# Kernel optimization log

Hardware: AMD Instinct MI355X
Metric: run time of the kernel (lower is better)

The kernel has to match this reference:

```python
import jax, jax.numpy as jnp
import numpy as np

N_NODES = 8192
DIM = 512

def setup_inputs() -> dict:
    key = jax.random.key(0)
    k1, k2, k3, k4 = jax.random.split(key, 4)
    x = jax.random.normal(k1, (N_NODES, DIM), dtype=jnp.float32)
    adj = jax.random.uniform(k2, (N_NODES, N_NODES), dtype=jnp.float32)
    # nn.Linear(dim, dim): weight [out, in], bias [out]
    bound = 1.0 / np.sqrt(DIM)
    W = jax.random.uniform(k3, (DIM, DIM), minval=-bound, maxval=bound, dtype=jnp.float32)
    b = jax.random.uniform(k4, (DIM,), minval=-bound, maxval=bound, dtype=jnp.float32)
    return {"x": x, "adj": adj, "W": W, "b": b}

def reference(x, adj, W, b):
    # agg = adj @ x : [N, dim]
    agg = jnp.matmul(adj, x)
    # Linear: agg @ W.T + b, then ReLU
    out = jnp.matmul(agg, W.T) + b
    return jax.nn.relu(out)
```

## Files before the change

kernel.cpp:

```cpp
#include <hip/hip_runtime.h>

typedef __bf16 bf16_t;
typedef bf16_t bf16x8 __attribute__((ext_vector_type(8)));
typedef bf16_t bf16x4 __attribute__((ext_vector_type(4)));
typedef float f32x4 __attribute__((ext_vector_type(4)));

#define N_NODES 8192
#define DIM 512

__global__ __launch_bounds__(256) void k_transpose_x(const float* __restrict__ x,
                                                     bf16_t* __restrict__ xT) {
  __shared__ float tile[64][65];
  const int m0 = blockIdx.x * 64;
  const int n0 = blockIdx.y * 64;
  const int t = threadIdx.x;
  const int r = t >> 4;
  const int c = (t & 15) << 2;
#pragma unroll
  for (int i = 0; i < 4; ++i) {
    f32x4 v = *(const f32x4*)&x[(size_t)(m0 + r + i * 16) * DIM + n0 + c];
    tile[r + i * 16][c + 0] = v.x;
    tile[r + i * 16][c + 1] = v.y;
    tile[r + i * 16][c + 2] = v.z;
    tile[r + i * 16][c + 3] = v.w;
  }
  __syncthreads();
#pragma unroll
  for (int i = 0; i < 4; ++i) {
    const int rn = r + i * 16;
    bf16x4 o = {(bf16_t)tile[c + 0][rn], (bf16_t)tile[c + 1][rn],
                (bf16_t)tile[c + 2][rn], (bf16_t)tile[c + 3][rn]};
    *(bf16x4*)&xT[(size_t)(n0 + rn) * N_NODES + m0 + c] = o;
  }
}

__global__ __launch_bounds__(256) void k_cvt_w(const float* __restrict__ W,
                                               bf16_t* __restrict__ Wb) {
  const int t = blockIdx.x * 256 + threadIdx.x;
  f32x4 v = *(const f32x4*)&W[(size_t)t * 4];
  bf16x4 o = {(bf16_t)v.x, (bf16_t)v.y, (bf16_t)v.z, (bf16_t)v.w};
  *(bf16x4*)&Wb[(size_t)t * 4] = o;
}

template <int S>
__global__ __launch_bounds__(512, 4) void k_gemm1(const float* __restrict__ A,
                                                  const bf16_t* __restrict__ Bt,
                                                  float* __restrict__ P) {
  constexpr int K = N_NODES;
  constexpr int KC = K / S;
  constexpr int NIT = KC / 32;
  constexpr int LD = 40;
  __shared__ bf16_t As[2][128 * LD];
  __shared__ bf16_t Bs[2][128 * LD];

  const int b = blockIdx.x;
  const int xcd = b & 7;
  const int i6 = b >> 3;
  const int n_tile = i6 & 3;
  const int s = (i6 >> 2) & (S - 1);
  const int mg = (i6 >> 2) / S;
  const int m0 = (mg * 8 + xcd) * 128;
  const int n0 = n_tile * 128;

  const int t = threadIdx.x;
  const int lane = t & 63;
  const int w = t >> 6;
  const int wr = w & 1;
  const int wc = w >> 1;
  const int lrow = lane & 15;
  const int quad = lane >> 4;
  const int sr = t >> 2;
  const int sq = t & 3;

  const float* ap = A + (size_t)(m0 + sr) * K + s * KC + sq * 8;
  const bf16_t* bp = Bt + (size_t)(n0 + sr) * K + s * KC + sq * 8;
  const int wofs = sr * LD + sq * 8;

  f32x4 pa0[2], pa1[2];
  bf16x8 pb[2];
  auto load_pre = [&](int k0, int sl) {
    pa0[sl] = *(const f32x4*)(ap + k0);
    pa1[sl] = *(const f32x4*)(ap + k0 + 4);
    pb[sl] = *(const bf16x8*)(bp + k0);
  };
  auto stage = [&](int sl, int buf) {
    bf16x8 av;
#pragma unroll
    for (int z = 0; z < 4; ++z) {
      av[z] = (bf16_t)pa0[sl][z];
      av[z + 4] = (bf16_t)pa1[sl][z];
    }
    *(bf16x8*)&As[buf][wofs] = av;
    *(bf16x8*)&Bs[buf][wofs] = pb[sl];
  };

  load_pre(0, 0);
  stage(0, 0);
  if (NIT > 1) load_pre(32, 1);
  f32x4 acc[4][2] = {};
  __syncthreads();

  int cur = 0;
#pragma unroll 2
  for (int it = 0; it < NIT; ++it) {
    if (it + 2 < NIT) load_pre((it + 2) * 32, it & 1);
    bf16x8 af[4], bfr[2];
#pragma unroll
    for (int ii = 0; ii < 4; ++ii)
      af[ii] = *(const bf16x8*)&As[cur][(wr * 64 + ii * 16 + lrow) * LD + quad * 8];
#pragma unroll
    for (int jj = 0; jj < 2; ++jj)
      bfr[jj] = *(const bf16x8*)&Bs[cur][(wc * 32 + jj * 16 + lrow) * LD + quad * 8];
#pragma unroll
    for (int ii = 0; ii < 4; ++ii)
#pragma unroll
      for (int jj = 0; jj < 2; ++jj)
        acc[ii][jj] = __builtin_amdgcn_mfma_f32_16x16x32_bf16(af[ii], bfr[jj], acc[ii][jj], 0, 0, 0);
    if (it + 1 < NIT) stage((it + 1) & 1, cur ^ 1);
    __syncthreads();
    cur ^= 1;
  }

  float* Pp = P + (size_t)s * N_NODES * DIM;
#pragma unroll
  for (int ii = 0; ii < 4; ++ii)
#pragma unroll
    for (int jj = 0; jj < 2; ++jj) {
      const int col = n0 + wc * 32 + jj * 16 + lrow;
#pragma unroll
      for (int r = 0; r < 4; ++r) {
        const int row = m0 + wr * 64 + ii * 16 + quad * 4 + r;
        Pp[(size_t)row * DIM + col] = acc[ii][jj][r];
      }
    }
}

template <int S>
__global__ __launch_bounds__(256, 2) void k_gemm2(const float* __restrict__ P,
                                                  const bf16_t* __restrict__ Bw,
                                                  const float* __restrict__ bias,
                                                  float* __restrict__ out) {
  constexpr int K = DIM;
  constexpr int LDA = 72;
  constexpr int LDB = 72;
  constexpr size_t PS = (size_t)N_NODES * DIM;
  __shared__ bf16_t As[64 * LDA];
  __shared__ bf16_t Bs[128 * LDB];

  const int b = blockIdx.x;
  const int n0 = (b & 3) * 128;
  const int m0 = (b >> 2) * 64;
  const int t = threadIdx.x;
  const int lane = t & 63;
  const int w = t >> 6;
  const int wr = w & 1;
  const int wc = w >> 1;
  const int lrow = lane & 15;
  const int quad = lane >> 4;
  const int ar = t >> 2, aq = t & 3;
  const int br = t >> 1, bq = t & 1;

  const float* ap = P + (size_t)(m0 + ar) * K + aq * 16;
  const bf16_t* bp = Bw + (size_t)(n0 + br) * K + bq * 32;
  bf16_t* aw = &As[ar * LDA + aq * 16];
  bf16_t* bw = &Bs[br * LDB + bq * 32];

  f32x4 acc[2][4] = {};

  for (int k0 = 0; k0 < K; k0 += 64) {
    f32x4 av[4];
#pragma unroll
    for (int z = 0; z < 4; ++z) av[z] = *(const f32x4*)(ap + k0 + z * 4);
#pragma unroll
    for (int s2 = 1; s2 < S; ++s2)
#pragma unroll
      for (int z = 0; z < 4; ++z) av[z] += *(const f32x4*)(ap + s2 * PS + k0 + z * 4);
    bf16x8 b0 = *(const bf16x8*)(bp + k0);
    bf16x8 b1 = *(const bf16x8*)(bp + k0 + 8);
    bf16x8 b2 = *(const bf16x8*)(bp + k0 + 16);
    bf16x8 b3 = *(const bf16x8*)(bp + k0 + 24);
    bf16x8 a0, a1;
#pragma unroll
    for (int z = 0; z < 4; ++z) {
      a0[z] = (bf16_t)av[0][z];
      a0[z + 4] = (bf16_t)av[1][z];
      a1[z] = (bf16_t)av[2][z];
      a1[z + 4] = (bf16_t)av[3][z];
    }
    __syncthreads();
    *(bf16x8*)aw = a0;
    *(bf16x8*)(aw + 8) = a1;
    *(bf16x8*)bw = b0;
    *(bf16x8*)(bw + 8) = b1;
    *(bf16x8*)(bw + 16) = b2;
    *(bf16x8*)(bw + 24) = b3;
    __syncthreads();
#pragma unroll
    for (int kk = 0; kk < 64; kk += 32) {
      bf16x8 af0 = *(const bf16x8*)&As[(wr * 32 + 0 + lrow) * LDA + kk + quad * 8];
      bf16x8 af1 = *(const bf16x8*)&As[(wr * 32 + 16 + lrow) * LDA + kk + quad * 8];
      bf16x8 bf0 = *(const bf16x8*)&Bs[(wc * 64 + 0 + lrow) * LDB + kk + quad * 8];
      bf16x8 bf1 = *(const bf16x8*)&Bs[(wc * 64 + 16 + lrow) * LDB + kk + quad * 8];
      bf16x8 bf2 = *(const bf16x8*)&Bs[(wc * 64 + 32 + lrow) * LDB + kk + quad * 8];
      bf16x8 bf3 = *(const bf16x8*)&Bs[(wc * 64 + 48 + lrow) * LDB + kk + quad * 8];
      acc[0][0] = __builtin_amdgcn_mfma_f32_16x16x32_bf16(af0, bf0, acc[0][0], 0, 0, 0);
      acc[0][1] = __builtin_amdgcn_mfma_f32_16x16x32_bf16(af0, bf1, acc[0][1], 0, 0, 0);
      acc[0][2] = __builtin_amdgcn_mfma_f32_16x16x32_bf16(af0, bf2, acc[0][2], 0, 0, 0);
      acc[0][3] = __builtin_amdgcn_mfma_f32_16x16x32_bf16(af0, bf3, acc[0][3], 0, 0, 0);
      acc[1][0] = __builtin_amdgcn_mfma_f32_16x16x32_bf16(af1, bf0, acc[1][0], 0, 0, 0);
      acc[1][1] = __builtin_amdgcn_mfma_f32_16x16x32_bf16(af1, bf1, acc[1][1], 0, 0, 0);
      acc[1][2] = __builtin_amdgcn_mfma_f32_16x16x32_bf16(af1, bf2, acc[1][2], 0, 0, 0);
      acc[1][3] = __builtin_amdgcn_mfma_f32_16x16x32_bf16(af1, bf3, acc[1][3], 0, 0, 0);
    }
  }

#pragma unroll
  for (int i = 0; i < 2; ++i)
#pragma unroll
    for (int j = 0; j < 4; ++j) {
      const int col = n0 + wc * 64 + j * 16 + lrow;
      const float bj = bias[col];
#pragma unroll
      for (int r = 0; r < 4; ++r) {
        const int row = m0 + wr * 32 + i * 16 + quad * 4 + r;
        float v = acc[i][j][r] + bj;
        out[(size_t)row * DIM + col] = v > 0.0f ? v : 0.0f;
      }
    }
}

extern "C" void kernel_launch(void* const* d_in, const int* in_sizes, int n_in,
                              void* d_out, int out_size, void* d_ws, size_t ws_size,
                              hipStream_t stream) {
  const float* x = (const float*)d_in[0];
  const float* adj = (const float*)d_in[1];
  const float* W = (const float*)d_in[2];
  const float* b = (const float*)d_in[3];
  float* out = (float*)d_out;

  bf16_t* xT = (bf16_t*)d_ws;
  bf16_t* Wb = xT + (size_t)DIM * N_NODES;
  float* P = (float*)(Wb + (size_t)DIM * DIM);
  const size_t base = (size_t)DIM * N_NODES * 2 + (size_t)DIM * DIM * 2;
  const size_t pslab = (size_t)N_NODES * DIM * 4;

  k_transpose_x<<<dim3(N_NODES / 64, DIM / 64), 256, 0, stream>>>(x, xT);
  k_cvt_w<<<dim3((DIM * DIM / 4) / 256), 256, 0, stream>>>(W, Wb);

  if (ws_size >= base + 4 * pslab) {
    k_gemm1<4><<<dim3(256 * 4), 512, 0, stream>>>(adj, xT, P);
    k_gemm2<4><<<dim3(512), 256, 0, stream>>>(P, Wb, b, out);
  } else {
    k_gemm1<1><<<dim3(256), 512, 0, stream>>>(adj, xT, P);
    k_gemm2<1><<<dim3(512), 256, 0, stream>>>(P, Wb, b, out);
  }
}
```

Baseline: 508.5 us.

## Stage gemm1 tiles via direct global-to-LDS loads with XOR swizzle and bigger warp tiles

```diff
diff --git a/kernel.cpp b/kernel.cpp
--- a/kernel.cpp
+++ b/kernel.cpp
@@ -1,4 +1,5 @@
 #include <hip/hip_runtime.h>
+#include <stdint.h>
 
 typedef __bf16 bf16_t;
 typedef bf16_t bf16x8 __attribute__((ext_vector_type(8)));
@@ -7,6 +8,13 @@
 
 #define N_NODES 8192
 #define DIM 512
+
+typedef __attribute__((address_space(1))) void as1_void;
+typedef __attribute__((address_space(3))) void as3_void;
+
+__device__ __forceinline__ void gload_lds16(const void* g, void* l) {
+  __builtin_amdgcn_global_load_lds((as1_void*)g, (as3_void*)l, 16, 0, 0);
+}
 
 __global__ __launch_bounds__(256) void k_transpose_x(const float* __restrict__ x,
                                                      bf16_t* __restrict__ xT) {
@@ -43,15 +51,14 @@
 }
 
 template <int S>
-__global__ __launch_bounds__(512, 4) void k_gemm1(const float* __restrict__ A,
+__global__ __launch_bounds__(256, 3) void k_gemm1(const float* __restrict__ A,
                                                   const bf16_t* __restrict__ Bt,
                                                   float* __restrict__ P) {
   constexpr int K = N_NODES;
   constexpr int KC = K / S;
   constexpr int NIT = KC / 32;
-  constexpr int LD = 40;
-  __shared__ bf16_t As[2][128 * LD];
-  __shared__ bf16_t Bs[2][128 * LD];
+  __shared__ float As[2][128 * 32];
+  __shared__ bf16_t Bs[2][128 * 32];
 
   const int b = blockIdx.x;
   const int xcd = b & 7;
@@ -69,64 +76,70 @@
   const int wc = w >> 1;
   const int lrow = lane & 15;
   const int quad = lane >> 4;
-  const int sr = t >> 2;
-  const int sq = t & 3;
-
-  const float* ap = A + (size_t)(m0 + sr) * K + s * KC + sq * 8;
-  const bf16_t* bp = Bt + (size_t)(n0 + sr) * K + s * KC + sq * 8;
-  const int wofs = sr * LD + sq * 8;
-
-  f32x4 pa0[2], pa1[2];
-  bf16x8 pb[2];
-  auto load_pre = [&](int k0, int sl) {
-    pa0[sl] = *(const f32x4*)(ap + k0);
-    pa1[sl] = *(const f32x4*)(ap + k0 + 4);
-    pb[sl] = *(const bf16x8*)(bp + k0);
+
+  const int aoff = ((t & 7) ^ ((t >> 3) & 7)) * 4;
+  const int boff = ((t & 3) ^ ((t >> 3) & 3)) * 8;
+  const float* ag = A + (size_t)(m0 + (t >> 3)) * K + (size_t)s * KC + aoff;
+  const bf16_t* bg = Bt + (size_t)(n0 + (t >> 2)) * K + (size_t)s * KC + boff;
+
+  auto stage = [&](int it, int buf) {
+    const int kc = it * 32;
+#pragma unroll
+    for (int i = 0; i < 4; ++i)
+      gload_lds16(ag + (size_t)(i * 32) * K + kc, &As[buf][(i * 256 + t) * 4]);
+#pragma unroll
+    for (int i = 0; i < 2; ++i)
+      gload_lds16(bg + (size_t)(i * 64) * K + kc, &Bs[buf][(i * 256 + t) * 8]);
   };
-  auto stage = [&](int sl, int buf) {
-    bf16x8 av;
-#pragma unroll
-    for (int z = 0; z < 4; ++z) {
-      av[z] = (bf16_t)pa0[sl][z];
-      av[z + 4] = (bf16_t)pa1[sl][z];
-    }
-    *(bf16x8*)&As[buf][wofs] = av;
-    *(bf16x8*)&Bs[buf][wofs] = pb[sl];
+
+  const int apc0 = ((quad * 2) ^ (lrow & 7)) * 4;
+  const int apc1 = (((quad * 2) ^ (lrow & 7)) ^ 1) * 4;
+  const int bpc = (quad ^ ((lrow >> 1) & 3)) * 8;
+
+  f32x4 acc[4][4] = {};
+
+  auto compute = [&](int buf) {
+    bf16x8 af[4], bfr[4];
+#pragma unroll
+    for (int ii = 0; ii < 4; ++ii) {
+      const int rb = (wr * 64 + ii * 16 + lrow) * 32;
+      f32x4 a0 = *(const f32x4*)&As[buf][rb + apc0];
+      f32x4 a1 = *(const f32x4*)&As[buf][rb + apc1];
+#pragma unroll
+      for (int z = 0; z < 4; ++z) {
+        af[ii][z] = (bf16_t)a0[z];
+        af[ii][z + 4] = (bf16_t)a1[z];
+      }
+    }
+#pragma unroll
+    for (int jj = 0; jj < 4; ++jj)
+      bfr[jj] = *(const bf16x8*)&Bs[buf][(wc * 64 + jj * 16 + lrow) * 32 + bpc];
+#pragma unroll
+    for (int ii = 0; ii < 4; ++ii)
+#pragma unroll
+      for (int jj = 0; jj < 4; ++jj)
+        acc[ii][jj] =
+            __builtin_amdgcn_mfma_f32_16x16x32_bf16(af[ii], bfr[jj], acc[ii][jj], 0, 0, 0);
   };
 
-  load_pre(0, 0);
   stage(0, 0);
-  if (NIT > 1) load_pre(32, 1);
-  f32x4 acc[4][2] = {};
   __syncthreads();
-
-  int cur = 0;
-#pragma unroll 2
-  for (int it = 0; it < NIT; ++it) {
-    if (it + 2 < NIT) load_pre((it + 2) * 32, it & 1);
-    bf16x8 af[4], bfr[2];
-#pragma unroll
-    for (int ii = 0; ii < 4; ++ii)
-      af[ii] = *(const bf16x8*)&As[cur][(wr * 64 + ii * 16 + lrow) * LD + quad * 8];
-#pragma unroll
-    for (int jj = 0; jj < 2; ++jj)
-      bfr[jj] = *(const bf16x8*)&Bs[cur][(wc * 32 + jj * 16 + lrow) * LD + quad * 8];
-#pragma unroll
-    for (int ii = 0; ii < 4; ++ii)
-#pragma unroll
-      for (int jj = 0; jj < 2; ++jj)
-        acc[ii][jj] = __builtin_amdgcn_mfma_f32_16x16x32_bf16(af[ii], bfr[jj], acc[ii][jj], 0, 0, 0);
-    if (it + 1 < NIT) stage((it + 1) & 1, cur ^ 1);
-    __syncthreads();
-    cur ^= 1;
+#pragma unroll 1
+  for (int it = 0; it < NIT; it += 2) {
+    stage(it + 1, 1);
+    compute(0);
+    __syncthreads();
+    if (it + 2 < NIT) stage(it + 2, 0);
+    compute(1);
+    __syncthreads();
   }
 
   float* Pp = P + (size_t)s * N_NODES * DIM;
 #pragma unroll
   for (int ii = 0; ii < 4; ++ii)
 #pragma unroll
-    for (int jj = 0; jj < 2; ++jj) {
-      const int col = n0 + wc * 32 + jj * 16 + lrow;
+    for (int jj = 0; jj < 4; ++jj) {
+      const int col = n0 + wc * 64 + jj * 16 + lrow;
 #pragma unroll
       for (int r = 0; r < 4; ++r) {
         const int row = m0 + wr * 64 + ii * 16 + quad * 4 + r;
@@ -148,8 +161,10 @@
   __shared__ bf16_t Bs[128 * LDB];
 
   const int b = blockIdx.x;
-  const int n0 = (b & 3) * 128;
-  const int m0 = (b >> 2) * 64;
+  const int xcd = b & 7;
+  const int j = b >> 3;
+  const int n0 = (j & 3) * 128;
+  const int m0 = ((j >> 2) * 8 + xcd) * 64;
   const int t = threadIdx.x;
   const int lane = t & 63;
   const int w = t >> 6;
@@ -217,13 +232,13 @@
 #pragma unroll
   for (int i = 0; i < 2; ++i)
 #pragma unroll
-    for (int j = 0; j < 4; ++j) {
-      const int col = n0 + wc * 64 + j * 16 + lrow;
+    for (int j2 = 0; j2 < 4; ++j2) {
+      const int col = n0 + wc * 64 + j2 * 16 + lrow;
       const float bj = bias[col];
 #pragma unroll
       for (int r = 0; r < 4; ++r) {
         const int row = m0 + wr * 32 + i * 16 + quad * 4 + r;
-        float v = acc[i][j][r] + bj;
+        float v = acc[i][j2][r] + bj;
         out[(size_t)row * DIM + col] = v > 0.0f ? v : 0.0f;
       }
     }
@@ -248,10 +263,10 @@
   k_cvt_w<<<dim3((DIM * DIM / 4) / 256), 256, 0, stream>>>(W, Wb);
 
   if (ws_size >= base + 4 * pslab) {
-    k_gemm1<4><<<dim3(256 * 4), 512, 0, stream>>>(adj, xT, P);
+    k_gemm1<4><<<dim3(256 * 4), 256, 0, stream>>>(adj, xT, P);
     k_gemm2<4><<<dim3(512), 256, 0, stream>>>(P, Wb, b, out);
   } else {
-    k_gemm1<1><<<dim3(256), 512, 0, stream>>>(adj, xT, P);
+    k_gemm1<1><<<dim3(256), 256, 0, stream>>>(adj, xT, P);
     k_gemm2<1><<<dim3(512), 256, 0, stream>>>(P, Wb, b, out);
   }
 }
```

After: 507.0 us. About the same (-0.3%).
